# Kernel tuning notes

Hardware: AMD Instinct MI355X
Metric: run time of the kernel (lower is better)

## Reference

```python
import jax, jax.numpy as jnp
import numpy as np

B, T, C, H = 2, 2048, 1024, 16
D = C // H  # head dim = 64

def setup_inputs() -> dict:
    key = jax.random.key(0)
    ks = jax.random.split(key, 5)
    s = 1.0 / np.sqrt(C)
    return {
        "x": jax.random.normal(ks[0], (B, T, C), jnp.float32),
        "Wq": jax.random.normal(ks[1], (C, C), jnp.float32) * s,
        "Wk": jax.random.normal(ks[2], (C, C), jnp.float32) * s,
        "Wv": jax.random.normal(ks[3], (C, C), jnp.float32) * s,
        "Wo": jax.random.normal(ks[4], (C, C), jnp.float32) * s,
    }

def reference(x, Wq, Wk, Wv, Wo):
    # torch Linear: y = x @ W.T  (weights stored [out, in])
    def proj(W):
        h = jnp.einsum('btc,oc->bto', x, W)
        return h.reshape(B, T, H, D).transpose(0, 2, 1, 3)  # [B,H,T,D]
    q, k, v = proj(Wq), proj(Wk), proj(Wv)
    scale = 1.0 / np.sqrt(D)
    att = jnp.einsum('bhqd,bhkd->bhqk', q, k) * scale  # [B,H,T,T]
    causal = jnp.tril(jnp.ones((T, T), bool))
    att = jnp.where(causal[None, None], att, -jnp.inf)
    att = jax.nn.softmax(att, axis=-1)
    y = jnp.einsum('bhqk,bhkd->bhqd', att, v)  # [B,H,T,D]
    y = y.transpose(0, 2, 1, 3).reshape(B, T, C)
    return jnp.einsum('btc,oc->bto', y, Wo)
```

## Files before the change

### kernel.cpp

```cpp
#include <hip/hip_runtime.h>
#include <math.h>

typedef short bf16x8 __attribute__((ext_vector_type(8)));
typedef float f32x4 __attribute__((ext_vector_type(4)));
typedef float f32x16 __attribute__((ext_vector_type(16)));
typedef int int2v __attribute__((ext_vector_type(2)));

constexpr int Bc = 2, Tc = 2048, Cc = 1024, Hc = 16, Dc = 64;
constexpr int Mc = Bc * Tc;

#if __has_builtin(__builtin_amdgcn_exp2f)
#define EXP2(x) __builtin_amdgcn_exp2f(x)
#else
#define EXP2(x) exp2f(x)
#endif

__device__ __forceinline__ unsigned short f2bf(float f) {
    union { float f; unsigned u; } v; v.f = f;
    unsigned r = v.u + 0x7fffu + ((v.u >> 16) & 1u);
    return (unsigned short)(r >> 16);
}

__device__ __forceinline__ unsigned cvt_pk_bf16(float lo, float hi) {
    unsigned r;
    asm("v_cvt_pk_bf16_f32 %0, %1, %2" : "=v"(r) : "v"(lo), "v"(hi));
    return r;
}

__device__ __forceinline__ void gload16(const void* g, void* l) {
    __builtin_amdgcn_global_load_lds(
        (const __attribute__((address_space(1))) void*)g,
        (__attribute__((address_space(3))) void*)l, 16, 0, 0);
}

__global__ __launch_bounds__(256)
void cast_bf16(const float* __restrict__ in, unsigned short* __restrict__ out, int n8) {
    int i = blockIdx.x * 256 + threadIdx.x;
    if (i >= n8) return;
    const float4* p = (const float4*)in;
    float4 a = p[i * 2], b = p[i * 2 + 1];
    union { unsigned short u[8]; bf16x8 v; } r;
    r.u[0] = f2bf(a.x); r.u[1] = f2bf(a.y); r.u[2] = f2bf(a.z); r.u[3] = f2bf(a.w);
    r.u[4] = f2bf(b.x); r.u[5] = f2bf(b.y); r.u[6] = f2bf(b.z); r.u[7] = f2bf(b.w);
    *(bf16x8*)(out + i * 8) = r.v;
}

__global__ __launch_bounds__(256)
void cast_w4(const float* __restrict__ a, const float* __restrict__ b,
             const float* __restrict__ c, const float* __restrict__ d,
             unsigned short* __restrict__ oa, unsigned short* __restrict__ ob,
             unsigned short* __restrict__ oc, unsigned short* __restrict__ od) {
    const float* src = blockIdx.y == 0 ? a : blockIdx.y == 1 ? b : blockIdx.y == 2 ? c : d;
    unsigned short* dst = blockIdx.y == 0 ? oa : blockIdx.y == 1 ? ob : blockIdx.y == 2 ? oc : od;
    int i = blockIdx.x * 256 + threadIdx.x;
    const float4* p = (const float4*)src;
    float4 x = p[i * 2], y = p[i * 2 + 1];
    union { unsigned short u[8]; bf16x8 v; } r;
    r.u[0] = f2bf(x.x); r.u[1] = f2bf(x.y); r.u[2] = f2bf(x.z); r.u[3] = f2bf(x.w);
    r.u[4] = f2bf(y.x); r.u[5] = f2bf(y.y); r.u[6] = f2bf(y.z); r.u[7] = f2bf(y.w);
    *(bf16x8*)(dst + i * 8) = r.v;
}

__global__ __launch_bounds__(256)
void gemm_qkv(const unsigned short* __restrict__ A,
              const unsigned short* __restrict__ Wq,
              const unsigned short* __restrict__ Wk,
              const unsigned short* __restrict__ Wv,
              unsigned short* __restrict__ Qo,
              unsigned short* __restrict__ Ko,
              unsigned short* __restrict__ Vo) {
    __shared__ unsigned short As[128 * 32];
    __shared__ unsigned short Bs[128 * 32];
    const int t = threadIdx.x;
    const int lane = t & 63, l15 = lane & 15, l4 = lane >> 4;
    const int w = t >> 6, wr = w >> 1, wc = w & 1;
    const int seg = blockIdx.y >> 3;
    const unsigned short* W = seg == 0 ? Wq : seg == 1 ? Wk : Wv;
    const int m0 = blockIdx.x * 128, n0 = (blockIdx.y & 7) * 128;

    f32x4 acc[4][4] = {};

    for (int k0 = 0; k0 < Cc; k0 += 32) {
        __syncthreads();
        #pragma unroll
        for (int it = 0; it < 2; ++it) {
            int c = t + it * 256;
            int row = c >> 2, ko = (c & 3) << 3;
            gload16(A + (size_t)(m0 + row) * Cc + k0 + ko, As + c * 8);
            gload16(W + (size_t)(n0 + row) * Cc + k0 + ko, Bs + c * 8);
        }
        __syncthreads();
        bf16x8 af[4], bfr[4];
        #pragma unroll
        for (int i = 0; i < 4; ++i)
            af[i] = *(const bf16x8*)(As + ((wr * 64 + i * 16 + l15) * 32 + l4 * 8));
        #pragma unroll
        for (int j = 0; j < 4; ++j)
            bfr[j] = *(const bf16x8*)(Bs + ((wc * 64 + j * 16 + l15) * 32 + l4 * 8));
        #pragma unroll
        for (int i = 0; i < 4; ++i)
            #pragma unroll
            for (int j = 0; j < 4; ++j)
                acc[i][j] = __builtin_amdgcn_mfma_f32_16x16x32_bf16(af[i], bfr[j], acc[i][j], 0, 0, 0);
    }

    const float qscale = 0.18033688011112042f;
    const int r0 = wr * 64 + (l4 << 2);
    const int c0 = wc * 64 + l15;
    #pragma unroll
    for (int i = 0; i < 4; ++i)
        #pragma unroll
        for (int j = 0; j < 4; ++j)
            #pragma unroll
            for (int r = 0; r < 4; ++r) {
                int row = m0 + r0 + i * 16 + r;
                int col = n0 + c0 + j * 16;
                float v = acc[i][j][r];
                int bb = row >> 11, tt = row & (Tc - 1);
                int hh = col >> 6, dd = col & 63;
                if (seg == 0)
                    Qo[((((size_t)bb * Hc + hh) * Tc + tt) << 6) + dd] = f2bf(v * qscale);
                else if (seg == 1)
                    Ko[((((size_t)bb * Hc + hh) * Tc + tt) << 6) + dd] = f2bf(v);
                else
                    Vo[(((size_t)bb * Hc + hh) * Dc + dd) * Tc + tt] = f2bf(v);
            }
}

__global__ __launch_bounds__(256)
void gemm_out(const unsigned short* __restrict__ A,
              const unsigned short* __restrict__ W,
              float* __restrict__ outp) {
    __shared__ unsigned short As[128 * 32];
    __shared__ unsigned short Bs[64 * 32];
    const int t = threadIdx.x;
    const int lane = t & 63, l15 = lane & 15, l4 = lane >> 4;
    const int w = t >> 6, wr = w >> 1, wc = w & 1;
    const int m0 = blockIdx.x * 128, n0 = blockIdx.y * 64;

    f32x4 acc[4][2] = {};

    for (int k0 = 0; k0 < Cc; k0 += 32) {
        __syncthreads();
        #pragma unroll
        for (int it = 0; it < 2; ++it) {
            int c = t + it * 256;
            int row = c >> 2, ko = (c & 3) << 3;
            gload16(A + (size_t)(m0 + row) * Cc + k0 + ko, As + c * 8);
        }
        {
            int c = t;
            int row = c >> 2, ko = (c & 3) << 3;
            gload16(W + (size_t)(n0 + row) * Cc + k0 + ko, Bs + c * 8);
        }
        __syncthreads();
        bf16x8 af[4], bfr[2];
        #pragma unroll
        for (int i = 0; i < 4; ++i)
            af[i] = *(const bf16x8*)(As + ((wr * 64 + i * 16 + l15) * 32 + l4 * 8));
        #pragma unroll
        for (int j = 0; j < 2; ++j)
            bfr[j] = *(const bf16x8*)(Bs + ((wc * 32 + j * 16 + l15) * 32 + l4 * 8));
        #pragma unroll
        for (int i = 0; i < 4; ++i)
            #pragma unroll
            for (int j = 0; j < 2; ++j)
                acc[i][j] = __builtin_amdgcn_mfma_f32_16x16x32_bf16(af[i], bfr[j], acc[i][j], 0, 0, 0);
    }

    const int r0 = wr * 64 + (l4 << 2);
    const int c0 = wc * 32 + l15;
    #pragma unroll
    for (int i = 0; i < 4; ++i)
        #pragma unroll
        for (int j = 0; j < 2; ++j)
            #pragma unroll
            for (int r = 0; r < 4; ++r)
                outp[(size_t)(m0 + r0 + i * 16 + r) * Cc + n0 + c0 + j * 16] = acc[i][j][r];
}

__global__ __launch_bounds__(256)
void attn_mfma(const unsigned short* __restrict__ Q,
               const unsigned short* __restrict__ K,
               const unsigned short* __restrict__ Vt,
               unsigned short* __restrict__ Y) {
    __shared__ unsigned short Ks[2][64 * 64];
    __shared__ unsigned short Vs[2][64 * 64];

    const int t = threadIdx.x, lane = t & 63, w = t >> 6;
    const int l31 = lane & 31, h = lane >> 5;
    const int qb = (int)gridDim.y - 1 - blockIdx.y;
    const int bh = blockIdx.x;
    const int bb = bh >> 4, hh = bh & 15;
    const int qbase = qb * 128 + w * 32;
    const int q = qbase + l31;

    const unsigned short* Qp = Q + (size_t)bh * Tc * Dc;
    const unsigned short* Kp = K + (size_t)bh * Tc * Dc;
    const unsigned short* Vp = Vt + (size_t)bh * Dc * Tc;

    bf16x8 qf[4];
    #pragma unroll
    for (int kc = 0; kc < 4; ++kc)
        qf[kc] = *(const bf16x8*)(Qp + (size_t)q * 64 + kc * 16 + h * 8);

    f32x16 ot[2] = {};
    float m = -INFINITY, lsum = 0.f;

    auto stage = [&](int kb, int buf) {
        #pragma unroll
        for (int it = 0; it < 2; ++it) {
            int c = t + it * 256;
            int row = c >> 3, slot = c & 7;
            int ss = slot ^ (row & 7);
            gload16(Kp + (size_t)(kb * 64 + row) * 64 + ss * 8, &Ks[buf][c * 8]);
            gload16(Vp + (size_t)row * Tc + kb * 64 + ss * 8, &Vs[buf][c * 8]);
        }
    };

    const int nkb = 2 * qb + 2;
    stage(0, 0);
    __syncthreads();

    for (int kb = 0; kb < nkb; ++kb) {
        const int cur = kb & 1;
        if (kb + 1 < nkb) stage(kb + 1, cur ^ 1);

        if (kb * 64 <= qbase + 31) {
            f32x16 st[2] = {};
            #pragma unroll
            for (int nt = 0; nt < 2; ++nt) {
                int key = nt * 32 + l31;
                #pragma unroll
                for (int kc = 0; kc < 4; ++kc) {
                    int boff = (kc * 32 + h * 16) ^ ((key & 7) << 4);
                    bf16x8 kf = *(const bf16x8*)(&Ks[cur][((key << 7) + boff) >> 1]);
                    st[nt] = __builtin_amdgcn_mfma_f32_32x32x16_bf16(kf, qf[kc], st[nt], 0, 0, 0);
                }
            }

            if (kb * 64 + 63 > qbase) {
                #pragma unroll
                for (int nt = 0; nt < 2; ++nt)
                    #pragma unroll
                    for (int r = 0; r < 16; ++r) {
                        int key = kb * 64 + nt * 32 + (r & 3) + 8 * (r >> 2) + 4 * h;
                        if (key > q) st[nt][r] = -1e30f;
                    }
            }

            float mx[16];
            #pragma unroll
            for (int r = 0; r < 16; ++r) mx[r] = fmaxf(st[0][r], st[1][r]);
            #pragma unroll
            for (int s2 = 8; s2 > 0; s2 >>= 1)
                #pragma unroll
                for (int r = 0; r < s2; ++r) mx[r] = fmaxf(mx[r], mx[r + s2]);
            float tmax = fmaxf(mx[0], __shfl_xor(mx[0], 32));

            if (__any(tmax > m + 8.f)) {
                float mn = fmaxf(m, tmax);
                float al = EXP2(m - mn);
                m = mn;
                lsum *= al;
                #pragma unroll
                for (int dt = 0; dt < 2; ++dt)
                    #pragma unroll
                    for (int r = 0; r < 16; ++r) ot[dt][r] *= al;
            }

            float ps = 0.f;
            #pragma unroll
            for (int nt = 0; nt < 2; ++nt)
                #pragma unroll
                for (int r = 0; r < 16; ++r) {
                    float p = EXP2(st[nt][r] - m);
                    st[nt][r] = p;
                    ps += p;
                }
            lsum += ps;

            #pragma unroll
            for (int nt = 0; nt < 2; ++nt) {
                unsigned a0 = cvt_pk_bf16(st[nt][0],  st[nt][1]);
                unsigned b0 = cvt_pk_bf16(st[nt][4],  st[nt][5]);
                unsigned a1 = cvt_pk_bf16(st[nt][2],  st[nt][3]);
                unsigned b1 = cvt_pk_bf16(st[nt][6],  st[nt][7]);
                int2v r0 = __builtin_amdgcn_permlane32_swap((int)a0, (int)b0, false, false);
                int2v r1 = __builtin_amdgcn_permlane32_swap((int)a1, (int)b1, false, false);
                union { unsigned u[4]; bf16x8 v; } pf0, pf1;
                pf0.u[0] = r0.x; pf0.u[1] = r1.x; pf0.u[2] = r0.y; pf0.u[3] = r1.y;
                unsigned c0 = cvt_pk_bf16(st[nt][8],  st[nt][9]);
                unsigned d0 = cvt_pk_bf16(st[nt][12], st[nt][13]);
                unsigned c1 = cvt_pk_bf16(st[nt][10], st[nt][11]);
                unsigned d1 = cvt_pk_bf16(st[nt][14], st[nt][15]);
                int2v r2 = __builtin_amdgcn_permlane32_swap((int)c0, (int)d0, false, false);
                int2v r3 = __builtin_amdgcn_permlane32_swap((int)c1, (int)d1, false, false);
                pf1.u[0] = r2.x; pf1.u[1] = r3.x; pf1.u[2] = r2.y; pf1.u[3] = r3.y;

                #pragma unroll
                for (int dt = 0; dt < 2; ++dt) {
                    int d = dt * 32 + l31;
                    int v0off = (nt * 64 + h * 16) ^ ((d & 7) << 4);
                    bf16x8 vf0 = *(const bf16x8*)(&Vs[cur][((d << 7) + v0off) >> 1]);
                    ot[dt] = __builtin_amdgcn_mfma_f32_32x32x16_bf16(vf0, pf0.v, ot[dt], 0, 0, 0);
                }
                #pragma unroll
                for (int dt = 0; dt < 2; ++dt) {
                    int d = dt * 32 + l31;
                    int v1off = (nt * 64 + 32 + h * 16) ^ ((d & 7) << 4);
                    bf16x8 vf1 = *(const bf16x8*)(&Vs[cur][((d << 7) + v1off) >> 1]);
                    ot[dt] = __builtin_amdgcn_mfma_f32_32x32x16_bf16(vf1, pf1.v, ot[dt], 0, 0, 0);
                }
            }
        }
        __syncthreads();
    }

    float lf = lsum + __shfl_xor(lsum, 32);
    float inv = 1.f / lf;
    size_t base = ((size_t)bb * Tc + q) * Cc + hh * 64;
    #pragma unroll
    for (int dt = 0; dt < 2; ++dt)
        #pragma unroll
        for (int rg = 0; rg < 4; ++rg) {
            int d0 = dt * 32 + rg * 8 + 4 * h;
            ushort4 s4;
            s4.x = f2bf(ot[dt][rg * 4 + 0] * inv);
            s4.y = f2bf(ot[dt][rg * 4 + 1] * inv);
            s4.z = f2bf(ot[dt][rg * 4 + 2] * inv);
            s4.w = f2bf(ot[dt][rg * 4 + 3] * inv);
            *(ushort4*)(Y + base + d0) = s4;
        }
}

extern "C" void kernel_launch(void* const* d_in, const int* in_sizes, int n_in,
                              void* d_out, int out_size, void* d_ws, size_t ws_size,
                              hipStream_t stream) {
    const float* x  = (const float*)d_in[0];
    const float* Wq = (const float*)d_in[1];
    const float* Wk = (const float*)d_in[2];
    const float* Wv = (const float*)d_in[3];
    const float* Wo = (const float*)d_in[4];

    unsigned short* ws = (unsigned short*)d_ws;
    const size_t nX = (size_t)Mc * Cc;
    const size_t nW = (size_t)Cc * Cc;
    size_t off = 0;
    unsigned short* xb  = ws + off; off += nX;
    unsigned short* Wqb = ws + off; off += nW;
    unsigned short* Wkb = ws + off; off += nW;
    unsigned short* Wvb = ws + off; off += nW;
    unsigned short* Wob = ws + off; off += nW;
    unsigned short* Qw  = ws + off; off += nX;
    unsigned short* Kw  = ws + off; off += nX;
    unsigned short* Vtw = ws + off; off += nX;
    unsigned short* Yb  = ws + off; off += nX;

    dim3 blk(256);
    cast_bf16<<<dim3((int)(nX / 8 / 256)), blk, 0, stream>>>(x, xb, (int)(nX / 8));
    cast_w4<<<dim3(512, 4), blk, 0, stream>>>(Wq, Wk, Wv, Wo, Wqb, Wkb, Wvb, Wob);

    gemm_qkv<<<dim3(Mc / 128, 24), blk, 0, stream>>>(xb, Wqb, Wkb, Wvb, Qw, Kw, Vtw);

    attn_mfma<<<dim3(Bc * Hc, Tc / 128), blk, 0, stream>>>(Qw, Kw, Vtw, Yb);

    gemm_out<<<dim3(Mc / 128, Cc / 64), blk, 0, stream>>>(Yb, Wob, (float*)d_out);
}
```

Before: 121.4 us.

## Split long causal attention rows across two blocks and merge with combine kernel

Attention blocks shrink to 64 queries with 128 threads, and a constant job table schedules work longest-first. Query tiles at positions 1024 and above are split into two key-range halves that write unnormalized partial outputs plus max and sum statistics, which a new combine kernel merges. This targets causal load imbalance and the tail effect of the old fixed 128-query grid. It also adds setprio around the MFMA sections and splits the row-sum accumulator into four parts. The costs are an extra kernel launch, extra global traffic for the partials, and reuse of the xb and Wqb workspace as scratch, which is only safe because those buffers are already consumed.

```diff
diff --git a/kernel.cpp b/kernel.cpp
--- a/kernel.cpp
+++ b/kernel.cpp
@@ -19,6 +19,10 @@
     union { float f; unsigned u; } v; v.f = f;
     unsigned r = v.u + 0x7fffu + ((v.u >> 16) & 1u);
     return (unsigned short)(r >> 16);
+}
+
+__device__ __forceinline__ float bf2f(unsigned short u) {
+    union { unsigned u; float f; } v; v.u = (unsigned)u << 16; return v.f;
 }
 
 __device__ __forceinline__ unsigned cvt_pk_bf16(float lo, float hi) {
@@ -179,20 +183,38 @@
                 outp[(size_t)(m0 + r0 + i * 16 + r) * Cc + n0 + c0 + j * 16] = acc[i][j][r];
 }
 
-__global__ __launch_bounds__(256)
+__device__ __constant__ unsigned char JOBS[48] = {
+    159, 223, 222, 15, 158, 157, 221, 220, 14, 156,
+    155, 219, 218, 13, 154, 153, 217, 216, 12, 152,
+    151, 215, 214, 11, 150, 149, 213, 212, 10, 148,
+    147, 211, 210,  9, 146, 145, 209, 208,  8, 144,
+      7,   6,   5,  4,   3,   2,   1,   0
+};
+
+__global__ __launch_bounds__(128)
 void attn_mfma(const unsigned short* __restrict__ Q,
                const unsigned short* __restrict__ K,
                const unsigned short* __restrict__ Vt,
-               unsigned short* __restrict__ Y) {
+               unsigned short* __restrict__ Y,
+               unsigned short* __restrict__ P1,
+               float* __restrict__ mlf) {
     __shared__ unsigned short Ks[2][64 * 64];
     __shared__ unsigned short Vs[2][64 * 64];
 
     const int t = threadIdx.x, lane = t & 63, w = t >> 6;
     const int l31 = lane & 31, h = lane >> 5;
-    const int qb = (int)gridDim.y - 1 - blockIdx.y;
     const int bh = blockIdx.x;
     const int bb = bh >> 4, hh = bh & 15;
-    const int qbase = qb * 128 + w * 32;
+
+    const unsigned char job = JOBS[blockIdx.y];
+    const int c = job & 31;
+    const bool split = job & 128;
+    const int half = (job >> 6) & 1;
+    const int ntile = c + 1, smid = ntile >> 1;
+    const int kb0 = (split && half) ? smid : 0;
+    const int kb1 = (split && !half) ? smid : ntile;
+
+    const int qbase = c * 64 + w * 32;
     const int q = qbase + l31;
 
     const unsigned short* Qp = Q + (size_t)bh * Tc * Dc;
@@ -209,116 +231,118 @@
 
     auto stage = [&](int kb, int buf) {
         #pragma unroll
-        for (int it = 0; it < 2; ++it) {
-            int c = t + it * 256;
-            int row = c >> 3, slot = c & 7;
+        for (int it = 0; it < 4; ++it) {
+            int idx = t + it * 128;
+            int row = idx >> 3, slot = idx & 7;
             int ss = slot ^ (row & 7);
-            gload16(Kp + (size_t)(kb * 64 + row) * 64 + ss * 8, &Ks[buf][c * 8]);
-            gload16(Vp + (size_t)row * Tc + kb * 64 + ss * 8, &Vs[buf][c * 8]);
+            gload16(Kp + (size_t)(kb * 64 + row) * 64 + ss * 8, &Ks[buf][idx * 8]);
+            gload16(Vp + (size_t)row * Tc + kb * 64 + ss * 8, &Vs[buf][idx * 8]);
         }
     };
 
-    const int nkb = 2 * qb + 2;
-    stage(0, 0);
+    stage(kb0, 0);
     __syncthreads();
 
-    for (int kb = 0; kb < nkb; ++kb) {
-        const int cur = kb & 1;
-        if (kb + 1 < nkb) stage(kb + 1, cur ^ 1);
-
-        if (kb * 64 <= qbase + 31) {
-            f32x16 st[2] = {};
-            #pragma unroll
-            for (int nt = 0; nt < 2; ++nt) {
-                int key = nt * 32 + l31;
-                #pragma unroll
-                for (int kc = 0; kc < 4; ++kc) {
-                    int boff = (kc * 32 + h * 16) ^ ((key & 7) << 4);
-                    bf16x8 kf = *(const bf16x8*)(&Ks[cur][((key << 7) + boff) >> 1]);
-                    st[nt] = __builtin_amdgcn_mfma_f32_32x32x16_bf16(kf, qf[kc], st[nt], 0, 0, 0);
-                }
+    for (int kb = kb0; kb < kb1; ++kb) {
+        const int cur = (kb - kb0) & 1;
+        if (kb + 1 < kb1) stage(kb + 1, cur ^ 1);
+
+        f32x16 st[2] = {};
+        __builtin_amdgcn_s_setprio(1);
+        #pragma unroll
+        for (int nt = 0; nt < 2; ++nt) {
+            int key = nt * 32 + l31;
+            #pragma unroll
+            for (int kc = 0; kc < 4; ++kc) {
+                int boff = (kc * 32 + h * 16) ^ ((key & 7) << 4);
+                bf16x8 kf = *(const bf16x8*)(&Ks[cur][((key << 7) + boff) >> 1]);
+                st[nt] = __builtin_amdgcn_mfma_f32_32x32x16_bf16(kf, qf[kc], st[nt], 0, 0, 0);
             }
-
-            if (kb * 64 + 63 > qbase) {
-                #pragma unroll
-                for (int nt = 0; nt < 2; ++nt)
-                    #pragma unroll
-                    for (int r = 0; r < 16; ++r) {
-                        int key = kb * 64 + nt * 32 + (r & 3) + 8 * (r >> 2) + 4 * h;
-                        if (key > q) st[nt][r] = -1e30f;
-                    }
-            }
-
-            float mx[16];
-            #pragma unroll
-            for (int r = 0; r < 16; ++r) mx[r] = fmaxf(st[0][r], st[1][r]);
-            #pragma unroll
-            for (int s2 = 8; s2 > 0; s2 >>= 1)
-                #pragma unroll
-                for (int r = 0; r < s2; ++r) mx[r] = fmaxf(mx[r], mx[r + s2]);
-            float tmax = fmaxf(mx[0], __shfl_xor(mx[0], 32));
-
-            if (__any(tmax > m + 8.f)) {
-                float mn = fmaxf(m, tmax);
-                float al = EXP2(m - mn);
-                m = mn;
-                lsum *= al;
-                #pragma unroll
-                for (int dt = 0; dt < 2; ++dt)
-                    #pragma unroll
-                    for (int r = 0; r < 16; ++r) ot[dt][r] *= al;
-            }
-
-            float ps = 0.f;
+        }
+        __builtin_amdgcn_s_setprio(0);
+
+        if (kb * 64 + 63 > qbase) {
             #pragma unroll
             for (int nt = 0; nt < 2; ++nt)
                 #pragma unroll
                 for (int r = 0; r < 16; ++r) {
-                    float p = EXP2(st[nt][r] - m);
-                    st[nt][r] = p;
-                    ps += p;
+                    int key = kb * 64 + nt * 32 + (r & 3) + 8 * (r >> 2) + 4 * h;
+                    if (key > q) st[nt][r] = -1e30f;
                 }
-            lsum += ps;
-
-            #pragma unroll
-            for (int nt = 0; nt < 2; ++nt) {
-                unsigned a0 = cvt_pk_bf16(st[nt][0],  st[nt][1]);
-                unsigned b0 = cvt_pk_bf16(st[nt][4],  st[nt][5]);
-                unsigned a1 = cvt_pk_bf16(st[nt][2],  st[nt][3]);
-                unsigned b1 = cvt_pk_bf16(st[nt][6],  st[nt][7]);
-                int2v r0 = __builtin_amdgcn_permlane32_swap((int)a0, (int)b0, false, false);
-                int2v r1 = __builtin_amdgcn_permlane32_swap((int)a1, (int)b1, false, false);
-                union { unsigned u[4]; bf16x8 v; } pf0, pf1;
-                pf0.u[0] = r0.x; pf0.u[1] = r1.x; pf0.u[2] = r0.y; pf0.u[3] = r1.y;
-                unsigned c0 = cvt_pk_bf16(st[nt][8],  st[nt][9]);
-                unsigned d0 = cvt_pk_bf16(st[nt][12], st[nt][13]);
-                unsigned c1 = cvt_pk_bf16(st[nt][10], st[nt][11]);
-                unsigned d1 = cvt_pk_bf16(st[nt][14], st[nt][15]);
-                int2v r2 = __builtin_amdgcn_permlane32_swap((int)c0, (int)d0, false, false);
-                int2v r3 = __builtin_amdgcn_permlane32_swap((int)c1, (int)d1, false, false);
-                pf1.u[0] = r2.x; pf1.u[1] = r3.x; pf1.u[2] = r2.y; pf1.u[3] = r3.y;
-
+        }
+
+        float mx[16];
+        #pragma unroll
+        for (int r = 0; r < 16; ++r) mx[r] = fmaxf(st[0][r], st[1][r]);
+        #pragma unroll
+        for (int s2 = 8; s2 > 0; s2 >>= 1)
+            #pragma unroll
+            for (int r = 0; r < s2; ++r) mx[r] = fmaxf(mx[r], mx[r + s2]);
+        float tmax = fmaxf(mx[0], __shfl_xor(mx[0], 32));
+
+        if (__any(tmax > m + 8.f)) {
+            float mn = fmaxf(m, tmax);
+            float al = EXP2(m - mn);
+            m = mn;
+            lsum *= al;
+            #pragma unroll
+            for (int dt = 0; dt < 2; ++dt)
                 #pragma unroll
-                for (int dt = 0; dt < 2; ++dt) {
-                    int d = dt * 32 + l31;
-                    int v0off = (nt * 64 + h * 16) ^ ((d & 7) << 4);
-                    bf16x8 vf0 = *(const bf16x8*)(&Vs[cur][((d << 7) + v0off) >> 1]);
-                    ot[dt] = __builtin_amdgcn_mfma_f32_32x32x16_bf16(vf0, pf0.v, ot[dt], 0, 0, 0);
-                }
-                #pragma unroll
-                for (int dt = 0; dt < 2; ++dt) {
-                    int d = dt * 32 + l31;
-                    int v1off = (nt * 64 + 32 + h * 16) ^ ((d & 7) << 4);
-                    bf16x8 vf1 = *(const bf16x8*)(&Vs[cur][((d << 7) + v1off) >> 1]);
-                    ot[dt] = __builtin_amdgcn_mfma_f32_32x32x16_bf16(vf1, pf1.v, ot[dt], 0, 0, 0);
-                }
+                for (int r = 0; r < 16; ++r) ot[dt][r] *= al;
+        }
+
+        float psa[4] = {0.f, 0.f, 0.f, 0.f};
+        #pragma unroll
+        for (int nt = 0; nt < 2; ++nt)
+            #pragma unroll
+            for (int r = 0; r < 16; ++r) {
+                float p = EXP2(st[nt][r] - m);
+                st[nt][r] = p;
+                psa[r & 3] += p;
             }
+        lsum += (psa[0] + psa[1]) + (psa[2] + psa[3]);
+
+        #pragma unroll
+        for (int nt = 0; nt < 2; ++nt) {
+            unsigned a0 = cvt_pk_bf16(st[nt][0],  st[nt][1]);
+            unsigned b0 = cvt_pk_bf16(st[nt][4],  st[nt][5]);
+            unsigned a1 = cvt_pk_bf16(st[nt][2],  st[nt][3]);
+            unsigned b1 = cvt_pk_bf16(st[nt][6],  st[nt][7]);
+            int2v r0 = __builtin_amdgcn_permlane32_swap((int)a0, (int)b0, false, false);
+            int2v r1 = __builtin_amdgcn_permlane32_swap((int)a1, (int)b1, false, false);
+            union { unsigned u[4]; bf16x8 v; } pf0, pf1;
+            pf0.u[0] = r0.x; pf0.u[1] = r1.x; pf0.u[2] = r0.y; pf0.u[3] = r1.y;
+            unsigned c0 = cvt_pk_bf16(st[nt][8],  st[nt][9]);
+            unsigned d0 = cvt_pk_bf16(st[nt][12], st[nt][13]);
+            unsigned c1 = cvt_pk_bf16(st[nt][10], st[nt][11]);
+            unsigned d1 = cvt_pk_bf16(st[nt][14], st[nt][15]);
+            int2v r2 = __builtin_amdgcn_permlane32_swap((int)c0, (int)d0, false, false);
+            int2v r3 = __builtin_amdgcn_permlane32_swap((int)c1, (int)d1, false, false);
+            pf1.u[0] = r2.x; pf1.u[1] = r3.x; pf1.u[2] = r2.y; pf1.u[3] = r3.y;
+
+            __builtin_amdgcn_s_setprio(1);
+            #pragma unroll
+            for (int dt = 0; dt < 2; ++dt) {
+                int d = dt * 32 + l31;
+                int v0off = (nt * 64 + h * 16) ^ ((d & 7) << 4);
+                bf16x8 vf0 = *(const bf16x8*)(&Vs[cur][((d << 7) + v0off) >> 1]);
+                ot[dt] = __builtin_amdgcn_mfma_f32_32x32x16_bf16(vf0, pf0.v, ot[dt], 0, 0, 0);
+            }
+            #pragma unroll
+            for (int dt = 0; dt < 2; ++dt) {
+                int d = dt * 32 + l31;
+                int v1off = (nt * 64 + 32 + h * 16) ^ ((d & 7) << 4);
+                bf16x8 vf1 = *(const bf16x8*)(&Vs[cur][((d << 7) + v1off) >> 1]);
+                ot[dt] = __builtin_amdgcn_mfma_f32_32x32x16_bf16(vf1, pf1.v, ot[dt], 0, 0, 0);
+            }
+            __builtin_amdgcn_s_setprio(0);
         }
         __syncthreads();
     }
 
     float lf = lsum + __shfl_xor(lsum, 32);
-    float inv = 1.f / lf;
+    unsigned short* dst = (split && half) ? P1 : Y;
+    float inv = split ? 1.f : 1.f / lf;
     size_t base = ((size_t)bb * Tc + q) * Cc + hh * 64;
     #pragma unroll
     for (int dt = 0; dt < 2; ++dt)
@@ -330,8 +354,38 @@
             s4.y = f2bf(ot[dt][rg * 4 + 1] * inv);
             s4.z = f2bf(ot[dt][rg * 4 + 2] * inv);
             s4.w = f2bf(ot[dt][rg * 4 + 3] * inv);
-            *(ushort4*)(Y + base + d0) = s4;
-        }
+            *(ushort4*)(dst + base + d0) = s4;
+        }
+    if (split && h == 0) {
+        int ridx = bh * 1024 + (q - 1024);
+        mlf[ridx + (half ? 65536 : 0)]          = m;
+        mlf[ridx + (half ? 98304 : 32768)]      = lf;
+    }
+}
+
+__global__ __launch_bounds__(256)
+void attn_combine(unsigned short* __restrict__ Y,
+                  const unsigned short* __restrict__ P1,
+                  const float* __restrict__ mlf) {
+    int tid = blockIdx.x * 256 + threadIdx.x;
+    int ridx = tid >> 3;
+    int d0 = (tid & 7) * 8;
+    int bh = ridx >> 10, qq = ridx & 1023;
+    int bb = bh >> 4, hh = bh & 15;
+    int q = 1024 + qq;
+    size_t off = ((size_t)bb * Tc + q) * Cc + hh * 64 + d0;
+    float m0 = mlf[ridx], l0 = mlf[ridx + 32768];
+    float m1 = mlf[ridx + 65536], l1 = mlf[ridx + 98304];
+    float M = fmaxf(m0, m1);
+    float a0 = exp2f(m0 - M), a1 = exp2f(m1 - M);
+    float inv = 1.f / (l0 * a0 + l1 * a1);
+    union { unsigned short u[8]; bf16x8 v; } y0, y1, r;
+    y0.v = *(const bf16x8*)(Y + off);
+    y1.v = *(const bf16x8*)(P1 + off);
+    #pragma unroll
+    for (int j = 0; j < 8; ++j)
+        r.u[j] = f2bf((bf2f(y0.u[j]) * a0 + bf2f(y1.u[j]) * a1) * inv);
+    *(bf16x8*)(Y + off) = r.v;
 }
 
 extern "C" void kernel_launch(void* const* d_in, const int* in_sizes, int n_in,
@@ -363,7 +417,10 @@
 
     gemm_qkv<<<dim3(Mc / 128, 24), blk, 0, stream>>>(xb, Wqb, Wkb, Wvb, Qw, Kw, Vtw);
 
-    attn_mfma<<<dim3(Bc * Hc, Tc / 128), blk, 0, stream>>>(Qw, Kw, Vtw, Yb);
+    unsigned short* P1 = xb;
+    float* mlf = (float*)Wqb;
+    attn_mfma<<<dim3(Bc * Hc, 48), dim3(128), 0, stream>>>(Qw, Kw, Vtw, Yb, P1, mlf);
+    attn_combine<<<dim3(1024), blk, 0, stream>>>(Yb, P1, mlf);
 
     gemm_out<<<dim3(Mc / 128, Cc / 64), blk, 0, stream>>>(Yb, Wob, (float*)d_out);
 }
```

After: 117.9 us. 1.03x faster.
